# Kernel optimization log

Hardware: AMD Instinct MI355X
Metric: run time of the kernel (lower is better)

## Reference

```python
import jax, jax.numpy as jnp
import numpy as np

H = 256  # hidden_dim
NH = 4   # num_heads
HD = H // NH  # head dim


def setup_inputs() -> dict:
    key = jax.random.key(0)
    ks = jax.random.split(key, 12)
    B, TD, ID = 65536, 512, 512
    s_t = 1.0 / np.sqrt(TD)
    s_h = 1.0 / np.sqrt(H)
    s_f = 1.0 / np.sqrt(2 * H)
    return {
        "text_features": jax.random.normal(ks[0], (B, TD), jnp.float32),
        "image_features": jax.random.normal(ks[1], (B, ID), jnp.float32),
        "W_text": jax.random.uniform(ks[2], (H, TD), jnp.float32, -s_t, s_t),
        "b_text": jax.random.uniform(ks[3], (H,), jnp.float32, -s_t, s_t),
        "W_img": jax.random.uniform(ks[4], (H, ID), jnp.float32, -s_t, s_t),
        "b_img": jax.random.uniform(ks[5], (H,), jnp.float32, -s_t, s_t),
        "in_proj_w": jax.random.normal(ks[6], (3 * H, H), jnp.float32) * s_h,  # xavier-ish
        "in_proj_b": jnp.zeros((3 * H,), jnp.float32),
        "out_proj_w": jax.random.uniform(ks[7], (H, H), jnp.float32, -s_h, s_h),
        "out_proj_b": jnp.zeros((H,), jnp.float32),
        "W_fuse": jax.random.uniform(ks[8], (H, 2 * H), jnp.float32, -s_f, s_f),
        "b_fuse": jax.random.uniform(ks[9], (H,), jnp.float32, -s_f, s_f),
    }


def _mha_seq1(q_in, kv_in, in_proj_w, in_proj_b, out_proj_w, out_proj_b):
    """nn.MultiheadAttention with query seq_len=1 and kv seq_len=1 (eval mode).
    q_in, kv_in: [B, H]. Softmax over the single key is identically 1."""
    Wq, Wk, Wv = jnp.split(in_proj_w, 3, axis=0)
    bq, bk, bv = jnp.split(in_proj_b, 3, axis=0)
    q = (q_in @ Wq.T + bq).reshape(-1, NH, HD)   # [B, nh, hd]
    k = (kv_in @ Wk.T + bk).reshape(-1, NH, HD)
    v = (kv_in @ Wv.T + bv).reshape(-1, NH, HD)
    scores = jnp.einsum("bnd,bnd->bn", q, k) / np.sqrt(HD)  # [B, nh], one key
    attn = jax.nn.softmax(scores[..., None], axis=-1)       # == 1 exactly
    out = (attn * v).reshape(-1, H)                          # concat heads
    return out @ out_proj_w.T + out_proj_b


def reference(text_features, image_features, W_text, b_text, W_img, b_img,
              in_proj_w, in_proj_b, out_proj_w, out_proj_b, W_fuse, b_fuse):
    tp = text_features @ W_text.T + b_text      # [B, H]
    ip = image_features @ W_img.T + b_img       # [B, H]
    text_att = _mha_seq1(tp, ip, in_proj_w, in_proj_b, out_proj_w, out_proj_b)
    img_att = _mha_seq1(ip, tp, in_proj_w, in_proj_b, out_proj_w, out_proj_b)
    fused = jnp.concatenate([text_att, img_att], axis=1)  # [B, 2H]
    return jax.nn.relu(fused @ W_fuse.T + b_fuse)          # dropout = eval no-op
```

## Files before the change

### kernel.cpp

```cpp
#include <hip/hip_runtime.h>
#include <hip/hip_bf16.h>

typedef __attribute__((ext_vector_type(4))) float floatx4;
typedef __attribute__((ext_vector_type(2))) float floatx2;
typedef __attribute__((ext_vector_type(8))) __bf16 bf16x8;
typedef __attribute__((ext_vector_type(8))) unsigned short ushortx8;

__device__ __forceinline__ unsigned short f2bf(float x) {
    union { float f; unsigned u; } v; v.f = x;
    unsigned r = v.u + 0x7fffu + ((v.u >> 16) & 1u);
    return (unsigned short)(r >> 16);
}

__device__ __forceinline__ bf16x8 as_bf(ushortx8 v) {
    union { ushortx8 u; bf16x8 b; } x; x.u = v; return x.b;
}

__device__ __forceinline__ bf16x8 cvt8(floatx4 lo, floatx4 hi) {
    union { bf16x8 v; __hip_bfloat162 h[4]; } u;
    float2 p;
    p.x = lo.x; p.y = lo.y; u.h[0] = __float22bfloat162_rn(p);
    p.x = lo.z; p.y = lo.w; u.h[1] = __float22bfloat162_rn(p);
    p.x = hi.x; p.y = hi.y; u.h[2] = __float22bfloat162_rn(p);
    p.x = hi.z; p.y = hi.w; u.h[3] = __float22bfloat162_rn(p);
    return u.v;
}

__global__ void k1_tree(const float* __restrict__ W_fuse, const float* __restrict__ OP,
                        const float* __restrict__ ipw, const float* __restrict__ ipb,
                        const float* __restrict__ W_img, const float* __restrict__ W_text,
                        const float* __restrict__ opb, const float* __restrict__ b_img,
                        const float* __restrict__ b_text,
                        float* __restrict__ U0, float* __restrict__ U1,
                        float* __restrict__ Vimg, float* __restrict__ Vtxt,
                        float* __restrict__ vb_img, float* __restrict__ vb_txt,
                        float* __restrict__ cvec) {
    const int bid = blockIdx.x;
    const int t = threadIdx.x;
    const float* Wv = ipw + 512 * 256;
    if (bid == 96) {
        if (t < 256) {
            float a0 = opb[t], a1 = 0.f, a2 = 0.f;
            const float* oprow = OP + t * 256;
            const float* wvrow = Wv + t * 256;
            #pragma unroll 4
            for (int k = 0; k < 256; ++k) {
                a0 = fmaf(oprow[k], ipb[512 + k], a0);
                a1 = fmaf(wvrow[k], b_img[k], a1);
                a2 = fmaf(wvrow[k], b_text[k], a2);
            }
            cvec[t] = a0; vb_img[t] = a1; vb_txt[t] = a2;
        }
        return;
    }
    const float *A, *B; float* C; int lda, ldb, ldc, aoff, tm, tn;
    if (bid < 32) {
        int h = bid >> 4, tt = bid & 15;
        A = W_fuse; lda = 512; aoff = h * 256;
        B = OP; ldb = 256; C = h ? U1 : U0; ldc = 256;
        tm = tt >> 2; tn = tt & 3;
    } else {
        int b2 = bid - 32; int h = b2 >> 5; int tt = b2 & 31;
        A = Wv; lda = 256; aoff = 0;
        B = h ? W_text : W_img; ldb = 512; C = h ? Vtxt : Vimg; ldc = 512;
        tm = tt >> 3; tn = tt & 7;
    }
    __shared__ float As[16][68];
    __shared__ float Bs[16][68];
    const int arow = t >> 3, ak = (t & 7) * 2;
    const int brow = t >> 5, bc = (t & 31) * 2;
    const int ty = t >> 4, tx = t & 15;
    float acc[2][4] = {};
    for (int k0 = 0; k0 < 256; k0 += 16) {
        floatx2 av = *(const floatx2*)(A + (size_t)(tm * 64 + arow) * lda + aoff + k0 + ak);
        floatx2 bv = *(const floatx2*)(B + (size_t)(k0 + brow) * ldb + tn * 64 + bc);
        __syncthreads();
        As[ak + 0][arow] = av.x;
        As[ak + 1][arow] = av.y;
        *(floatx2*)&Bs[brow][bc] = bv;
        __syncthreads();
        #pragma unroll
        for (int kk = 0; kk < 16; ++kk) {
            floatx2 a = *(const floatx2*)&As[kk][ty * 2];
            floatx4 b = *(const floatx4*)&Bs[kk][tx * 4];
            acc[0][0] = fmaf(a.x, b.x, acc[0][0]); acc[0][1] = fmaf(a.x, b.y, acc[0][1]);
            acc[0][2] = fmaf(a.x, b.z, acc[0][2]); acc[0][3] = fmaf(a.x, b.w, acc[0][3]);
            acc[1][0] = fmaf(a.y, b.x, acc[1][0]); acc[1][1] = fmaf(a.y, b.y, acc[1][1]);
            acc[1][2] = fmaf(a.y, b.z, acc[1][2]); acc[1][3] = fmaf(a.y, b.w, acc[1][3]);
        }
    }
    #pragma unroll
    for (int i = 0; i < 2; ++i) {
        floatx4 o; o.x = acc[i][0]; o.y = acc[i][1]; o.z = acc[i][2]; o.w = acc[i][3];
        *(floatx4*)(C + (size_t)(tm * 64 + ty * 2 + i) * ldc + tn * 64 + tx * 4) = o;
    }
}

__global__ void k2_A(const float* __restrict__ U0, const float* __restrict__ U1,
                     const float* __restrict__ Vimg, const float* __restrict__ Vtxt,
                     const float* __restrict__ W_fuse, const float* __restrict__ b_fuse,
                     const float* __restrict__ vb_img, const float* __restrict__ vb_txt,
                     const float* __restrict__ cvec,
                     unsigned short* __restrict__ Wt, float* __restrict__ b_total) {
    const int bid = blockIdx.x;
    const int t = threadIdx.x;
    if (bid == 64) {
        if (t < 256) {
            float acc = b_fuse[t];
            const float* u0 = U0 + t * 256;
            const float* u1 = U1 + t * 256;
            const float* wf = W_fuse + t * 512;
            #pragma unroll 4
            for (int j = 0; j < 256; ++j) {
                acc = fmaf(u0[j], vb_img[j], acc);
                acc = fmaf(u1[j], vb_txt[j], acc);
                acc = fmaf(wf[j] + wf[j + 256], cvec[j], acc);
            }
            b_total[t] = acc;
        }
        return;
    }
    const int h = bid >> 5, tt = bid & 31;
    const float* A = h ? U1 : U0;
    const float* B = h ? Vtxt : Vimg;
    const int tm = tt >> 3, tn = tt & 7;
    __shared__ float As[16][68];
    __shared__ float Bs[16][68];
    const int arow = t >> 3, ak = (t & 7) * 2;
    const int brow = t >> 5, bc = (t & 31) * 2;
    const int n_l = t >> 3, oct = t & 7;
    float acc[8] = {};
    for (int k0 = 0; k0 < 256; k0 += 16) {
        floatx2 av = *(const floatx2*)(A + (size_t)(tm * 64 + arow) * 256 + k0 + ak);
        floatx2 bv = *(const floatx2*)(B + (size_t)(k0 + brow) * 512 + tn * 64 + bc);
        __syncthreads();
        As[ak + 0][arow] = av.x;
        As[ak + 1][arow] = av.y;
        *(floatx2*)&Bs[brow][bc] = bv;
        __syncthreads();
        #pragma unroll
        for (int kk = 0; kk < 16; ++kk) {
            float u = As[kk][n_l];
            floatx4 v0 = *(const floatx4*)&Bs[kk][oct * 8];
            floatx4 v1 = *(const floatx4*)&Bs[kk][oct * 8 + 4];
            acc[0] = fmaf(u, v0.x, acc[0]); acc[1] = fmaf(u, v0.y, acc[1]);
            acc[2] = fmaf(u, v0.z, acc[2]); acc[3] = fmaf(u, v0.w, acc[3]);
            acc[4] = fmaf(u, v1.x, acc[4]); acc[5] = fmaf(u, v1.y, acc[5]);
            acc[6] = fmaf(u, v1.z, acc[6]); acc[7] = fmaf(u, v1.w, acc[7]);
        }
    }
    const int n = tm * 64 + n_l;
    const int kg = h * 512 + tn * 64 + oct * 8;
    const int kq = kg >> 5, q = (kg >> 3) & 3;
    const int nt = n >> 4, nl = n & 15;
    union { ushortx8 v; unsigned short s[8]; } o;
    #pragma unroll
    for (int j = 0; j < 8; ++j) o.s[j] = f2bf(acc[j]);
    *(ushortx8*)&Wt[(size_t)((nt * 32 + kq) * 64 + q * 16 + nl) * 8] = o.v;
}

__global__ __launch_bounds__(256, 4)
void fused_gemm(const float* __restrict__ Ximg, const float* __restrict__ Xtxt,
                const unsigned short* __restrict__ Wt,
                const float* __restrict__ b_total, float* __restrict__ out) {
    const int t = threadIdx.x, lane = t & 63, w = t >> 6;
    const int ml = lane & 15, q = lane >> 4;
    const size_t rowbase = (size_t)blockIdx.x * 32;

    floatx4 acc[2][4];
    #pragma unroll
    for (int mi = 0; mi < 2; ++mi)
        #pragma unroll
        for (int ni = 0; ni < 4; ++ni) acc[mi][ni] = (floatx4){0.f, 0.f, 0.f, 0.f};

    const unsigned short* wt_lane = Wt + lane * 8;

    #pragma unroll 1
    for (int s = 0; s < 4; ++s) {
        const float* X = (s < 2) ? Ximg : Xtxt;
        const int koff = (s & 1) * 256;
        const float* pa0 = X + (rowbase + ml) * 512 + koff + q * 8;
        #pragma unroll
        for (int kqi = 0; kqi < 8; ++kqi) {
            const int kq = s * 8 + kqi;
            bf16x8 af[2];
            #pragma unroll
            for (int mi = 0; mi < 2; ++mi) {
                const float* p = pa0 + (size_t)mi * 16 * 512 + kqi * 32;
                floatx4 lo = *(const floatx4*)p;
                floatx4 hi = *(const floatx4*)(p + 4);
                af[mi] = cvt8(lo, hi);
            }
            #pragma unroll
            for (int ni = 0; ni < 4; ++ni) {
                ushortx8 bv = *(const ushortx8*)(wt_lane + (size_t)((w * 4 + ni) * 32 + kq) * 512);
                #pragma unroll
                for (int mi = 0; mi < 2; ++mi)
                    acc[mi][ni] = __builtin_amdgcn_mfma_f32_16x16x32_bf16(af[mi], as_bf(bv), acc[mi][ni], 0, 0, 0);
            }
        }
    }

    #pragma unroll
    for (int ni = 0; ni < 4; ++ni) {
        const int col = w * 64 + ni * 16 + ml;
        const float bias = b_total[col];
        #pragma unroll
        for (int mi = 0; mi < 2; ++mi) {
            const size_t r0 = rowbase + mi * 16 + q * 4;
            #pragma unroll
            for (int e = 0; e < 4; ++e) {
                float v = acc[mi][ni][e] + bias;
                out[(r0 + e) * 256 + col] = fmaxf(v, 0.f);
            }
        }
    }
}

extern "C" void kernel_launch(void* const* d_in, const int* in_sizes, int n_in,
                              void* d_out, int out_size, void* d_ws, size_t ws_size,
                              hipStream_t stream) {
    const float* text       = (const float*)d_in[0];
    const float* image      = (const float*)d_in[1];
    const float* W_text     = (const float*)d_in[2];
    const float* b_text     = (const float*)d_in[3];
    const float* W_img      = (const float*)d_in[4];
    const float* b_img      = (const float*)d_in[5];
    const float* in_proj_w  = (const float*)d_in[6];
    const float* in_proj_b  = (const float*)d_in[7];
    const float* out_proj_w = (const float*)d_in[8];
    const float* out_proj_b = (const float*)d_in[9];
    const float* W_fuse     = (const float*)d_in[10];
    const float* b_fuse     = (const float*)d_in[11];
    float* out = (float*)d_out;

    float* ws      = (float*)d_ws;
    float* U0      = ws;
    float* U1      = ws + 65536;
    float* Vimg    = ws + 131072;
    float* Vtxt    = ws + 262144;
    float* vb_img  = ws + 393216;
    float* vb_txt  = ws + 393472;
    float* cvec    = ws + 393728;
    float* b_total = ws + 393984;
    unsigned short* Wt = (unsigned short*)(ws + 394240);

    k1_tree<<<dim3(97), dim3(512), 0, stream>>>(W_fuse, out_proj_w, in_proj_w, in_proj_b,
                                                W_img, W_text, out_proj_b, b_img, b_text,
                                                U0, U1, Vimg, Vtxt, vb_img, vb_txt, cvec);
    k2_A<<<dim3(65), dim3(512), 0, stream>>>(U0, U1, Vimg, Vtxt, W_fuse, b_fuse,
                                             vb_img, vb_txt, cvec, Wt, b_total);
    fused_gemm<<<dim3(2048), dim3(256), 0, stream>>>(image, text, Wt, b_total, out);
}
```

Measured before the change: 470.9 us.

## Stage activation tiles through double-buffered LDS with register prefetch

```diff
diff --git a/kernel.cpp b/kernel.cpp
--- a/kernel.cpp
+++ b/kernel.cpp
@@ -16,8 +16,8 @@
     union { ushortx8 u; bf16x8 b; } x; x.u = v; return x.b;
 }
 
-__device__ __forceinline__ bf16x8 cvt8(floatx4 lo, floatx4 hi) {
-    union { bf16x8 v; __hip_bfloat162 h[4]; } u;
+__device__ __forceinline__ ushortx8 cvt8u(floatx4 lo, floatx4 hi) {
+    union { ushortx8 v; __hip_bfloat162 h[4]; } u;
     float2 p;
     p.x = lo.x; p.y = lo.y; u.h[0] = __float22bfloat162_rn(p);
     p.x = lo.z; p.y = lo.w; u.h[1] = __float22bfloat162_rn(p);
@@ -163,9 +163,12 @@
 void fused_gemm(const float* __restrict__ Ximg, const float* __restrict__ Xtxt,
                 const unsigned short* __restrict__ Wt,
                 const float* __restrict__ b_total, float* __restrict__ out) {
+    __shared__ unsigned short lds[2][32 * 264];
     const int t = threadIdx.x, lane = t & 63, w = t >> 6;
     const int ml = lane & 15, q = lane >> 4;
     const size_t rowbase = (size_t)blockIdx.x * 32;
+    const int sr = t >> 3;
+    const int sc = (t & 7) * 32;
 
     floatx4 acc[2][4];
     #pragma unroll
@@ -173,31 +176,50 @@
         #pragma unroll
         for (int ni = 0; ni < 4; ++ni) acc[mi][ni] = (floatx4){0.f, 0.f, 0.f, 0.f};
 
-    const unsigned short* wt_lane = Wt + lane * 8;
-
-    #pragma unroll 1
-    for (int s = 0; s < 4; ++s) {
+    floatx4 lr[8];
+
+    auto load_regs = [&](int s) {
         const float* X = (s < 2) ? Ximg : Xtxt;
-        const int koff = (s & 1) * 256;
-        const float* pa0 = X + (rowbase + ml) * 512 + koff + q * 8;
+        const float* gp = X + (rowbase + sr) * 512 + (s & 1) * 256 + sc;
+        #pragma unroll
+        for (int i = 0; i < 8; ++i) lr[i] = *(const floatx4*)(gp + i * 4);
+    };
+    auto write_stage = [&](int b) {
+        unsigned short* lp = &lds[b][sr * 264 + sc];
+        #pragma unroll
+        for (int j = 0; j < 4; ++j)
+            *(ushortx8*)(lp + j * 8) = cvt8u(lr[2 * j], lr[2 * j + 1]);
+    };
+    auto compute = [&](int s, int b) {
         #pragma unroll
         for (int kqi = 0; kqi < 8; ++kqi) {
             const int kq = s * 8 + kqi;
             bf16x8 af[2];
             #pragma unroll
             for (int mi = 0; mi < 2; ++mi) {
-                const float* p = pa0 + (size_t)mi * 16 * 512 + kqi * 32;
-                floatx4 lo = *(const floatx4*)p;
-                floatx4 hi = *(const floatx4*)(p + 4);
-                af[mi] = cvt8(lo, hi);
+                const unsigned short* ap = &lds[b][(mi * 16 + ml) * 264 + kqi * 32 + q * 8];
+                af[mi] = as_bf(*(const ushortx8*)ap);
             }
             #pragma unroll
             for (int ni = 0; ni < 4; ++ni) {
-                ushortx8 bv = *(const ushortx8*)(wt_lane + (size_t)((w * 4 + ni) * 32 + kq) * 512);
+                ushortx8 bv = *(const ushortx8*)(Wt + (size_t)(((w * 4 + ni) * 32 + kq) * 64 + lane) * 8);
                 #pragma unroll
                 for (int mi = 0; mi < 2; ++mi)
                     acc[mi][ni] = __builtin_amdgcn_mfma_f32_16x16x32_bf16(af[mi], as_bf(bv), acc[mi][ni], 0, 0, 0);
             }
+        }
+    };
+
+    load_regs(0);
+    write_stage(0);
+    __syncthreads();
+    #pragma unroll
+    for (int s = 0; s < 4; ++s) {
+        if (s < 3) load_regs(s + 1);
+        compute(s, s & 1);
+        if (s < 3) {
+            write_stage((s + 1) & 1);
+            __syncthreads();
         }
     }
 
```

Result: faster. 398.7 us (-15.3%).
